# Kernel optimization log

Hardware: AMD Instinct MI355X
Metric: run time of the kernel (lower is better)

## Reference

```python
import jax, jax.numpy as jnp
import numpy as np
from jax import lax

POOL = 2  # pool_kernel

def _conv2d(x, w, b, stride=1):
    # x: [N,C,H,W], w: [O,I,kh,kw] (torch OIHW layout)
    y = lax.conv_general_dilated(
        x, w, window_strides=(stride, stride), padding='VALID',
        dimension_numbers=('NCHW', 'OIHW', 'NCHW'))
    return y + b[None, :, None, None]

def _maxpool(x, k):
    return lax.reduce_window(x, -jnp.inf, lax.max,
                             (1, 1, k, k), (1, 1, k, k), 'VALID')

def setup_inputs() -> dict:
    key = jax.random.key(0)
    ks = jax.random.split(key, 8)
    B, S, D = 8, 64, 128
    C = 32  # num_channels, depth=3 -> channels 1->32->64->64
    def kaiming(k, shape):
        fan_in = shape[1] * shape[2] * shape[3]
        return jax.random.normal(k, shape, jnp.float32) * np.float32(np.sqrt(2.0 / fan_in))
    return {
        'token_features': jax.random.normal(ks[0], (B, S, D), jnp.float32),
        'type_embedds': jax.random.normal(ks[1], (B, S, D), jnp.float32),
        'w0': kaiming(ks[2], (C, 1, 3, 3)),
        'b0': jnp.zeros((C,), jnp.float32),
        'w1': kaiming(ks[3], (2 * C, C, 3, 3)),
        'b1': jnp.zeros((2 * C,), jnp.float32),
        'w2': kaiming(ks[4], (2 * C, 2 * C, 3, 3)),
        'b2': jnp.zeros((2 * C,), jnp.float32),
    }

def reference(token_features, type_embedds, w0, b0, w1, b1, w2, b2):
    B, S, D = type_embedds.shape
    # Outter2dFusion: ger(gate, features) -> fused[b,s,i,j] = type[b,s,i]*token[b,s,j]
    fused = jnp.einsum('bsi,bsj->bsij', type_embedds, token_features)
    x = fused.reshape(B * S, 1, D, D)  # each token's d x d map as 1-channel image
    gelu = lambda t: jax.nn.gelu(t, approximate=False)  # torch GELU default (erf)
    x = _maxpool(gelu(_conv2d(x, w0, b0, stride=1)), POOL)
    x = _maxpool(gelu(_conv2d(x, w1, b1, stride=1)), POOL)
    x = _maxpool(gelu(_conv2d(x, w2, b2, stride=1)), POOL)
    # dropout is identity at inference
    return x.reshape(B, S, -1)
```

## Files before the change

### kernel.cpp

```cpp
#include <hip/hip_runtime.h>


typedef short short8 __attribute__((ext_vector_type(8)));
typedef float f32x4 __attribute__((ext_vector_type(4)));

#define OFF_TY   0
#define OFF_HLO  512
#define OFF_HHI  16640
#define OFF_P0   24704
#define OFF_P1   41600
#define OFF_TK   OFF_P1
#define LDS_TOTAL (41600 + 1472*16)

__device__ __forceinline__ unsigned short f2bf(float f) {
    unsigned int u = __float_as_uint(f);
    u += 0x7fffu + ((u >> 16) & 1u);
    return (unsigned short)(u >> 16);
}

__device__ __forceinline__ float gelu_f(float x) {
    float ax = __builtin_fabsf(x);
    float E  = __builtin_amdgcn_exp2f(x * x * -0.72134752f);
    float k  = __builtin_amdgcn_rcpf(__builtin_fmaf(0.33267686f, ax, 1.0f));
    float s  = __builtin_fmaf(0.7478556f, k, -0.0958798f);
    s = __builtin_fmaf(s, k, 0.3480242f);
    s = s * k;
    float erfabs = __builtin_fmaf(-s, E, 1.0f);
    return __builtin_fmaf(0.5f * ax, erfabs, 0.5f * x);
}

__device__ __forceinline__ void produce(char* smem, const float* tys,
                                        float b0r, int c, int tid, int R0) {
    float t0 = tys[2*R0+0], t1 = tys[2*R0+1], t2 = tys[2*R0+2],
          t3 = tys[2*R0+3], t4 = tys[2*R0+4], t5 = tys[2*R0+5];
    int rest = tid >> 5;
    #pragma unroll
    for (int k = 0; k < 8; ++k, rest += 16) {
        if (rest < 126) {
            int roff = (rest >= 63) ? 1 : 0;
            int q = rest - (roff ? 63 : 0);
            float s0 = roff ? t2 : t0;
            float s1 = roff ? t3 : t1;
            float s2 = roff ? t4 : t2;
            float s3 = roff ? t5 : t3;
            uint2 lo = *(const uint2*)(smem + OFF_HLO + (c*126 + 2*q)*4);
            unsigned int hi = *(const unsigned int*)(smem + OFF_HHI + (c*126 + 2*q)*2);
            float h00 = __uint_as_float(lo.x << 16);
            float h10 = __uint_as_float(lo.x & 0xffff0000u);
            float h01 = __uint_as_float(lo.y << 16);
            float h11 = __uint_as_float(lo.y & 0xffff0000u);
            float h20 = __uint_as_float(hi << 16);
            float h21 = __uint_as_float(hi & 0xffff0000u);
            float e00 = __builtin_fmaf(s0,h00, __builtin_fmaf(s1,h10, __builtin_fmaf(s2,h20, b0r)));
            float e10 = __builtin_fmaf(s1,h00, __builtin_fmaf(s2,h10, __builtin_fmaf(s3,h20, b0r)));
            float e01 = __builtin_fmaf(s0,h01, __builtin_fmaf(s1,h11, __builtin_fmaf(s2,h21, b0r)));
            float e11 = __builtin_fmaf(s1,h01, __builtin_fmaf(s2,h11, __builtin_fmaf(s3,h21, b0r)));
            float m = gelu_f(fmaxf(fmaxf(e00, e01), fmaxf(e10, e11)));
            int slot = (R0 + roff) & 3;
            int unit = slot*264 + (q>>1)*8 + ((4*(q&1) + (c>>3)) ^ ((q>>1)&7));
            *(unsigned short*)(smem + OFF_P0 + unit*16 + (c&7)*2) = f2bf(m);
        }
    }
}

__attribute__((amdgpu_waves_per_eu(4)))
__launch_bounds__(512, 2)
__global__ void conv_pipeline(const float* __restrict__ token,
                              const float* __restrict__ type_,
                              const float* __restrict__ w0, const float* __restrict__ b0,
                              const float* __restrict__ w1, const float* __restrict__ b1,
                              const float* __restrict__ w2, const float* __restrict__ b2,
                              float* __restrict__ out) {
    extern __shared__ char smem[];
    float* tys = (float*)(smem + OFF_TY);
    float* tks = (float*)(smem + OFF_TK);

    const int tid = threadIdx.x;
    const int img = blockIdx.x;
    const int w   = tid >> 6;
    const int l   = tid & 63;
    const int l15 = l & 15;
    const int lc  = l >> 4;
    const int c0w = tid & 31;

    for (int i = tid; i < 128; i += 512) {
        tys[i] = type_[img*128 + i];
        tks[i] = token[img*128 + i];
    }

    const float b0r = b0[c0w];

    __syncthreads();

    {
        float w0r[9];
        #pragma unroll
        for (int i = 0; i < 9; ++i) w0r[i] = w0[c0w*9 + i];
        int x = tid >> 5;
        #pragma unroll
        for (int k = 0; k < 8; ++k, x += 16) {
            if (x < 126) {
                float t0 = tks[x], t1 = tks[x+1], t2 = tks[x+2];
                float h0 = __builtin_fmaf(w0r[0],t0, __builtin_fmaf(w0r[1],t1, w0r[2]*t2));
                float h1 = __builtin_fmaf(w0r[3],t0, __builtin_fmaf(w0r[4],t1, w0r[5]*t2));
                float h2 = __builtin_fmaf(w0r[6],t0, __builtin_fmaf(w0r[7],t1, w0r[8]*t2));
                unsigned int lov = (unsigned int)f2bf(h0) | ((unsigned int)f2bf(h1) << 16);
                *(unsigned int*)(smem + OFF_HLO + (c0w*126 + x)*4) = lov;
                *(unsigned short*)(smem + OFF_HHI + (c0w*126 + x)*2) = f2bf(h2);
            }
        }
    }

    short8 wf[18];
    float bias;
    const int ch = ((w & 3) * 16) + l15;
    if (w < 4) {
        bias = b1[ch];
        #pragma unroll
        for (int uv = 0; uv < 9; ++uv) {
            short8 f;
            #pragma unroll
            for (int j = 0; j < 8; ++j)
                f[j] = (short)f2bf(w1[(ch*32 + 8*lc + j)*9 + uv]);
            wf[uv] = f;
        }
    } else {
        bias = b2[ch];
        #pragma unroll
        for (int kh = 0; kh < 2; ++kh)
            #pragma unroll
            for (int uv = 0; uv < 9; ++uv) {
                short8 f;
                #pragma unroll
                for (int j = 0; j < 8; ++j)
                    f[j] = (short)f2bf(w2[(ch*64 + kh*32 + 8*lc + j)*9 + uv]);
                wf[kh*9 + uv] = f;
            }
    }

    __syncthreads();

    produce(smem, tys, b0r, c0w, tid, 0);
    produce(smem, tys, b0r, c0w, tid, 2);

    const size_t obase = (size_t)img * 12544;

    f32x4 acc[4];

    for (int i1 = 0; i1 < 30; ++i1) {
        __syncthreads();

        if (w < 4) {
            int rbase = (i1 % 6) * 30;
            int xr = ch >> 3;
            #pragma unroll
            for (int half = 0; half < 2; ++half) {
                #pragma unroll
                for (int i = 0; i < 4; ++i) acc[i] = (f32x4){0.f,0.f,0.f,0.f};
                #pragma unroll
                for (int pr = 0; pr < 4; ++pr) {
                    int sbase = ((2*i1 + pr) & 3) * 264;
                    #pragma unroll
                    for (int v = 0; v < 3; ++v) {
                        #pragma unroll
                        for (int mtl = 0; mtl < 2; ++mtl) {
                            int col = (2*half + mtl)*16 + l15 + v;
                            int unit = sbase + (col>>1)*8 + ((4*(col&1) + lc) ^ ((col>>1)&7));
                            short8 a = *(const short8*)(smem + OFF_P0 + unit*16);
                            if (pr <= 2)
                                acc[mtl*2+0] = __builtin_amdgcn_mfma_f32_16x16x32_bf16(
                                    a, wf[pr*3+v], acc[mtl*2+0], 0, 0, 0);
                            if (pr >= 1)
                                acc[mtl*2+1] = __builtin_amdgcn_mfma_f32_16x16x32_bf16(
                                    a, wf[(pr-1)*3+v], acc[mtl*2+1], 0, 0, 0);
                        }
                    }
                }
                #pragma unroll
                for (int mtl = 0; mtl < 2; ++mtl) {
                    int pcol = (2*half + mtl)*8 + lc*2;
                    if (pcol < 30) {
                        f32x4 A0 = acc[mtl*2+0], A1 = acc[mtl*2+1];
                        float p0 = fmaxf(fmaxf(A0[0], A0[1]), fmaxf(A1[0], A1[1]));
                        float p1 = fmaxf(fmaxf(A0[2], A0[3]), fmaxf(A1[2], A1[3]));
                        float m0 = gelu_f(p0 + bias);
                        float m1 = gelu_f(p1 + bias);
                        int u0 = (rbase + pcol)*8     + (xr ^ (pcol & 7));
                        int u1 = (rbase + pcol + 1)*8 + (xr ^ ((pcol+1) & 7));
                        *(unsigned short*)(smem + OFF_P1 + u0*16 + (ch&7)*2) = f2bf(m0);
                        *(unsigned short*)(smem + OFF_P1 + u1*16 + (ch&7)*2) = f2bf(m1);
                    }
                }
            }
        } else if (i1 >= 4 && (i1 & 1) == 0) {
            const int i2 = (i1 - 4) >> 1;
            #pragma unroll
            for (int i = 0; i < 4; ++i) acc[i] = (f32x4){0.f,0.f,0.f,0.f};
            #pragma unroll
            for (int pr = 0; pr < 4; ++pr) {
                int rb = ((2*i2 + pr) % 6) * 30;
                #pragma unroll
                for (int v = 0; v < 3; ++v) {
                    #pragma unroll
                    for (int mt = 0; mt < 2; ++mt) {
                        int col = mt*16 + l15 + v;
                        #pragma unroll
                        for (int kh = 0; kh < 2; ++kh) {
                            int unit = (rb + col)*8 + ((kh*4 + lc) ^ (col & 7));
                            short8 a = *(const short8*)(smem + OFF_P1 + unit*16);
                            if (pr <= 2)
                                acc[mt*2+0] = __builtin_amdgcn_mfma_f32_16x16x32_bf16(
                                    a, wf[kh*9 + pr*3+v], acc[mt*2+0], 0, 0, 0);
                            if (pr >= 1)
                                acc[mt*2+1] = __builtin_amdgcn_mfma_f32_16x16x32_bf16(
                                    a, wf[kh*9 + (pr-1)*3+v], acc[mt*2+1], 0, 0, 0);
                        }
                    }
                }
            }
            #pragma unroll
            for (int mt = 0; mt < 2; ++mt) {
                int pcol = mt*8 + lc*2;
                if (pcol < 14) {
                    f32x4 A0 = acc[mt*2+0], A1 = acc[mt*2+1];
                    float g00 = gelu_f(A0[0] + bias), g01 = gelu_f(A0[1] + bias);
                    float g02 = gelu_f(A0[2] + bias), g03 = gelu_f(A0[3] + bias);
                    float g10 = gelu_f(A1[0] + bias), g11 = gelu_f(A1[1] + bias);
                    float g12 = gelu_f(A1[2] + bias), g13 = gelu_f(A1[3] + bias);
                    float m0 = fmaxf(fmaxf(g00, g01), fmaxf(g10, g11));
                    float m1 = fmaxf(fmaxf(g02, g03), fmaxf(g12, g13));
                    float2 st; st.x = m0; st.y = m1;
                    *(float2*)(out + obase + ch*196 + i2*14 + pcol) = st;
                }
            }
        }

        __syncthreads();
        if (i1 < 29) produce(smem, tys, b0r, c0w, tid, 2*i1 + 4);
    }

    __syncthreads();
    if (w >= 4) {
        const int i2 = 13;
        #pragma unroll
        for (int i = 0; i < 4; ++i) acc[i] = (f32x4){0.f,0.f,0.f,0.f};
        #pragma unroll
        for (int pr = 0; pr < 4; ++pr) {
            int rb = ((2*i2 + pr) % 6) * 30;
            #pragma unroll
            for (int v = 0; v < 3; ++v) {
                #pragma unroll
                for (int mt = 0; mt < 2; ++mt) {
                    int col = mt*16 + l15 + v;
                    #pragma unroll
                    for (int kh = 0; kh < 2; ++kh) {
                        int unit = (rb + col)*8 + ((kh*4 + lc) ^ (col & 7));
                        short8 a = *(const short8*)(smem + OFF_P1 + unit*16);
                        if (pr <= 2)
                            acc[mt*2+0] = __builtin_amdgcn_mfma_f32_16x16x32_bf16(
                                a, wf[kh*9 + pr*3+v], acc[mt*2+0], 0, 0, 0);
                        if (pr >= 1)
                            acc[mt*2+1] = __builtin_amdgcn_mfma_f32_16x16x32_bf16(
                                a, wf[kh*9 + (pr-1)*3+v], acc[mt*2+1], 0, 0, 0);
                    }
                }
            }
        }
        #pragma unroll
        for (int mt = 0; mt < 2; ++mt) {
            int pcol = mt*8 + lc*2;
            if (pcol < 14) {
                f32x4 A0 = acc[mt*2+0], A1 = acc[mt*2+1];
                float g00 = gelu_f(A0[0] + bias), g01 = gelu_f(A0[1] + bias);
                float g02 = gelu_f(A0[2] + bias), g03 = gelu_f(A0[3] + bias);
                float g10 = gelu_f(A1[0] + bias), g11 = gelu_f(A1[1] + bias);
                float g12 = gelu_f(A1[2] + bias), g13 = gelu_f(A1[3] + bias);
                float m0 = fmaxf(fmaxf(g00, g01), fmaxf(g10, g11));
                float m1 = fmaxf(fmaxf(g02, g03), fmaxf(g12, g13));
                float2 st; st.x = m0; st.y = m1;
                *(float2*)(out + obase + ch*196 + i2*14 + pcol) = st;
            }
        }
    }
}

extern "C" void kernel_launch(void* const* d_in, const int* in_sizes, int n_in,
                              void* d_out, int out_size, void* d_ws, size_t ws_size,
                              hipStream_t stream) {
    const float* token = (const float*)d_in[0];
    const float* type_ = (const float*)d_in[1];
    const float* w0 = (const float*)d_in[2];
    const float* b0 = (const float*)d_in[3];
    const float* w1 = (const float*)d_in[4];
    const float* b1 = (const float*)d_in[5];
    const float* w2 = (const float*)d_in[6];
    const float* b2 = (const float*)d_in[7];
    float* out = (float*)d_out;

    hipLaunchKernelGGL(conv_pipeline, dim3(512), dim3(512), LDS_TOTAL, stream,
                       token, type_, w0, b0, w1, b1, w2, b2, out);
}
```

Before: 225.8 us.

## Interleave conv0 production with MFMA conv1/conv2 work using six-slot ring buffer

The stage-0 pooled rows were previously produced after a barrier in a separate phase, with a four-slot ring. They are now produced in chunks interleaved between MFMA groups inside the conv1 and conv2 loops, or by idle waves, and the P0 ring grows to six slots so the rows being written do not overlap the rows being read. This removes one barrier per iteration and lets VALU work overlap matrix work. In exchange it uses more LDS, which may affect the two-blocks-per-CU occupancy, and it drops the waves_per_eu attribute.

```diff
diff --git a/kernel.cpp b/kernel.cpp
--- a/kernel.cpp
+++ b/kernel.cpp
@@ -8,9 +8,9 @@
 #define OFF_HLO  512
 #define OFF_HHI  16640
 #define OFF_P0   24704
-#define OFF_P1   41600
+#define OFF_P1   50048
 #define OFF_TK   OFF_P1
-#define LDS_TOTAL (41600 + 1472*16)
+#define LDS_TOTAL (50048 + 23552)
 
 __device__ __forceinline__ unsigned short f2bf(float f) {
     unsigned int u = __float_as_uint(f);
@@ -29,41 +29,36 @@
     return __builtin_fmaf(0.5f * ax, erfabs, 0.5f * x);
 }
 
-__device__ __forceinline__ void produce(char* smem, const float* tys,
-                                        float b0r, int c, int tid, int R0) {
-    float t0 = tys[2*R0+0], t1 = tys[2*R0+1], t2 = tys[2*R0+2],
-          t3 = tys[2*R0+3], t4 = tys[2*R0+4], t5 = tys[2*R0+5];
-    int rest = tid >> 5;
-    #pragma unroll
-    for (int k = 0; k < 8; ++k, rest += 16) {
-        if (rest < 126) {
-            int roff = (rest >= 63) ? 1 : 0;
-            int q = rest - (roff ? 63 : 0);
-            float s0 = roff ? t2 : t0;
-            float s1 = roff ? t3 : t1;
-            float s2 = roff ? t4 : t2;
-            float s3 = roff ? t5 : t3;
-            uint2 lo = *(const uint2*)(smem + OFF_HLO + (c*126 + 2*q)*4);
-            unsigned int hi = *(const unsigned int*)(smem + OFF_HHI + (c*126 + 2*q)*2);
-            float h00 = __uint_as_float(lo.x << 16);
-            float h10 = __uint_as_float(lo.x & 0xffff0000u);
-            float h01 = __uint_as_float(lo.y << 16);
-            float h11 = __uint_as_float(lo.y & 0xffff0000u);
-            float h20 = __uint_as_float(hi << 16);
-            float h21 = __uint_as_float(hi & 0xffff0000u);
-            float e00 = __builtin_fmaf(s0,h00, __builtin_fmaf(s1,h10, __builtin_fmaf(s2,h20, b0r)));
-            float e10 = __builtin_fmaf(s1,h00, __builtin_fmaf(s2,h10, __builtin_fmaf(s3,h20, b0r)));
-            float e01 = __builtin_fmaf(s0,h01, __builtin_fmaf(s1,h11, __builtin_fmaf(s2,h21, b0r)));
-            float e11 = __builtin_fmaf(s1,h01, __builtin_fmaf(s2,h11, __builtin_fmaf(s3,h21, b0r)));
-            float m = gelu_f(fmaxf(fmaxf(e00, e01), fmaxf(e10, e11)));
-            int slot = (R0 + roff) & 3;
-            int unit = slot*264 + (q>>1)*8 + ((4*(q&1) + (c>>3)) ^ ((q>>1)&7));
-            *(unsigned short*)(smem + OFF_P0 + unit*16 + (c&7)*2) = f2bf(m);
-        }
-    }
-}
-
-__attribute__((amdgpu_waves_per_eu(4)))
+__device__ __forceinline__ void produce_chunk(char* smem,
+                                              float t0, float t1, float t2,
+                                              float t3, float t4, float t5,
+                                              float b0r, int c, int rest, int R0) {
+    if (rest < 126) {
+        int roff = (rest >= 63) ? 1 : 0;
+        int q = rest - (roff ? 63 : 0);
+        float s0 = roff ? t2 : t0;
+        float s1 = roff ? t3 : t1;
+        float s2 = roff ? t4 : t2;
+        float s3 = roff ? t5 : t3;
+        uint2 lo = *(const uint2*)(smem + OFF_HLO + (c*126 + 2*q)*4);
+        unsigned int hi = *(const unsigned int*)(smem + OFF_HHI + (c*126 + 2*q)*2);
+        float h00 = __uint_as_float(lo.x << 16);
+        float h10 = __uint_as_float(lo.x & 0xffff0000u);
+        float h01 = __uint_as_float(lo.y << 16);
+        float h11 = __uint_as_float(lo.y & 0xffff0000u);
+        float h20 = __uint_as_float(hi << 16);
+        float h21 = __uint_as_float(hi & 0xffff0000u);
+        float e00 = __builtin_fmaf(s0,h00, __builtin_fmaf(s1,h10, __builtin_fmaf(s2,h20, b0r)));
+        float e10 = __builtin_fmaf(s1,h00, __builtin_fmaf(s2,h10, __builtin_fmaf(s3,h20, b0r)));
+        float e01 = __builtin_fmaf(s0,h01, __builtin_fmaf(s1,h11, __builtin_fmaf(s2,h21, b0r)));
+        float e11 = __builtin_fmaf(s1,h01, __builtin_fmaf(s2,h11, __builtin_fmaf(s3,h21, b0r)));
+        float m = gelu_f(fmaxf(fmaxf(e00, e01), fmaxf(e10, e11)));
+        int slot = (R0 + roff) % 6;
+        int unit = slot*264 + (q>>1)*8 + ((4*(q&1) + (c>>3)) ^ ((q>>1)&7));
+        *(unsigned short*)(smem + OFF_P0 + unit*16 + (c&7)*2) = f2bf(m);
+    }
+}
+
 __launch_bounds__(512, 2)
 __global__ void conv_pipeline(const float* __restrict__ token,
                               const float* __restrict__ type_,
@@ -82,6 +77,7 @@
     const int l15 = l & 15;
     const int lc  = l >> 4;
     const int c0w = tid & 31;
+    const int rest0 = tid >> 5;
 
     for (int i = tid; i < 128; i += 512) {
         tys[i] = type_[img*128 + i];
@@ -140,26 +136,42 @@
 
     __syncthreads();
 
-    produce(smem, tys, b0r, c0w, tid, 0);
-    produce(smem, tys, b0r, c0w, tid, 2);
+    {
+        float t0 = tys[0], t1 = tys[1], t2 = tys[2],
+              t3 = tys[3], t4 = tys[4], t5 = tys[5];
+        #pragma unroll
+        for (int k = 0; k < 8; ++k)
+            produce_chunk(smem, t0,t1,t2,t3,t4,t5, b0r, c0w, rest0 + 16*k, 0);
+        t0 = tys[4]; t1 = tys[5]; t2 = tys[6];
+        t3 = tys[7]; t4 = tys[8]; t5 = tys[9];
+        #pragma unroll
+        for (int k = 0; k < 8; ++k)
+            produce_chunk(smem, t0,t1,t2,t3,t4,t5, b0r, c0w, rest0 + 16*k, 2);
+    }
+    __syncthreads();
 
     const size_t obase = (size_t)img * 12544;
 
-    f32x4 acc[4];
-
     for (int i1 = 0; i1 < 30; ++i1) {
-        __syncthreads();
+        const int doP = (i1 < 29);
+        const int R0p = 2*i1 + 4;
+        float t0, t1, t2, t3, t4, t5;
+        if (doP) {
+            t0 = tys[2*R0p+0]; t1 = tys[2*R0p+1]; t2 = tys[2*R0p+2];
+            t3 = tys[2*R0p+3]; t4 = tys[2*R0p+4]; t5 = tys[2*R0p+5];
+        }
 
         if (w < 4) {
             int rbase = (i1 % 6) * 30;
             int xr = ch >> 3;
             #pragma unroll
             for (int half = 0; half < 2; ++half) {
+                f32x4 acc[4];
                 #pragma unroll
                 for (int i = 0; i < 4; ++i) acc[i] = (f32x4){0.f,0.f,0.f,0.f};
                 #pragma unroll
                 for (int pr = 0; pr < 4; ++pr) {
-                    int sbase = ((2*i1 + pr) & 3) * 264;
+                    int sbase = ((2*i1 + pr) % 6) * 264;
                     #pragma unroll
                     for (int v = 0; v < 3; ++v) {
                         #pragma unroll
@@ -175,6 +187,8 @@
                                     a, wf[(pr-1)*3+v], acc[mtl*2+1], 0, 0, 0);
                         }
                     }
+                    if (doP) produce_chunk(smem, t0,t1,t2,t3,t4,t5, b0r, c0w,
+                                           rest0 + 16*(half*4 + pr), R0p);
                 }
                 #pragma unroll
                 for (int mtl = 0; mtl < 2; ++mtl) {
@@ -194,6 +208,7 @@
             }
         } else if (i1 >= 4 && (i1 & 1) == 0) {
             const int i2 = (i1 - 4) >> 1;
+            f32x4 acc[4];
             #pragma unroll
             for (int i = 0; i < 4; ++i) acc[i] = (f32x4){0.f,0.f,0.f,0.f};
             #pragma unroll
@@ -217,6 +232,10 @@
                         }
                     }
                 }
+                if (doP) {
+                    produce_chunk(smem, t0,t1,t2,t3,t4,t5, b0r, c0w, rest0 + 16*(2*pr),   R0p);
+                    produce_chunk(smem, t0,t1,t2,t3,t4,t5, b0r, c0w, rest0 + 16*(2*pr+1), R0p);
+                }
             }
             #pragma unroll
             for (int mt = 0; mt < 2; ++mt) {
@@ -233,15 +252,20 @@
                     *(float2*)(out + obase + ch*196 + i2*14 + pcol) = st;
                 }
             }
+        } else {
+            if (doP) {
+                #pragma unroll
+                for (int k = 0; k < 8; ++k)
+                    produce_chunk(smem, t0,t1,t2,t3,t4,t5, b0r, c0w, rest0 + 16*k, R0p);
+            }
         }
 
         __syncthreads();
-        if (i1 < 29) produce(smem, tys, b0r, c0w, tid, 2*i1 + 4);
-    }
-
-    __syncthreads();
+    }
+
     if (w >= 4) {
         const int i2 = 13;
+        f32x4 acc[4];
         #pragma unroll
         for (int i = 0; i < 4; ++i) acc[i] = (f32x4){0.f,0.f,0.f,0.f};
         #pragma unroll
```

After: 192.6 us. 14.7% less time.
